# Kernel optimization log

Hardware: AMD Instinct MI355X
Metric: run time of the kernel (lower is better)

Reference implementation:

```python
import jax, jax.numpy as jnp
import numpy as np

PAD_IDX = 0
K = 5
TEMPERATURE = 1.0
BATCH = 256
VOCAB = 50257


def setup_inputs() -> dict:
    key = jax.random.key(0)
    k1, k2, k3, k4, k5 = jax.random.split(key, 5)
    draft_tokens = jax.random.randint(k1, (BATCH, K), 0, VOCAB)
    # valid-ish log-probabilities (negative values)
    draft_log_probs = -jax.random.uniform(k2, (BATCH, K), minval=0.05, maxval=8.0, dtype=jnp.float32)
    target_logits = jax.random.normal(k3, (BATCH, K, VOCAB), dtype=jnp.float32)
    random_vals = jax.random.uniform(k4, (BATCH, K), dtype=jnp.float32)
    uniform_sample = jax.random.uniform(k5, (BATCH,), dtype=jnp.float32)
    return {
        "draft_tokens": draft_tokens,
        "draft_log_probs": draft_log_probs,
        "target_logits": target_logits,
        "random_vals": random_vals,
        "uniform_sample": uniform_sample,
    }


def reference(draft_tokens, draft_log_probs, target_logits, random_vals, uniform_sample):
    B, k = draft_tokens.shape
    # --- accept/reject scan ---
    tlp = jax.nn.log_softmax(target_logits / TEMPERATURE, axis=-1)          # [B,k,V]
    tlp_draft = jnp.take_along_axis(tlp, draft_tokens[..., None], axis=2)[..., 0]  # [B,k]
    accept_probs = jnp.minimum(jnp.exp(tlp_draft - draft_log_probs), 1.0)
    accepted_mask = random_vals < accept_probs
    rejected_sent = jnp.concatenate(
        [~accepted_mask, jnp.ones((B, 1), dtype=bool)], axis=1)              # [B,k+1]
    first_reject = jnp.argmax(rejected_sent, axis=1)                         # [B]
    n_accepted = first_reject
    # fixed-width (k) accepted_tokens, PAD-filled past n_accepted (jit-friendly
    # variant of torch's dynamic max_accepted truncation; same valid entries)
    pos = jnp.arange(k)[None, :]
    accepted_tokens = jnp.where(pos < n_accepted[:, None], draft_tokens, PAD_IDX)
    # --- vectorized fallback sampling at first reject position ---
    rp = jnp.minimum(first_reject, k - 1)                                    # clamp for gather
    sel_logits = jnp.take_along_axis(target_logits, rp[:, None, None], axis=1)[:, 0, :]  # [B,V]
    target_probs = jax.nn.softmax(sel_logits / TEMPERATURE, axis=-1)
    dlp_sel = jnp.take_along_axis(draft_log_probs, rp[:, None], axis=1)      # [B,1]
    # torch builds a constant vector exp(dlp) over the whole vocab
    draft_probs = jnp.exp(dlp_sel)                                           # [B,1] broadcasts
    adjusted = jnp.clip(target_probs - draft_probs, 0.0)
    s = adjusted.sum(axis=-1, keepdims=True)
    probs = jnp.where(s > 0, adjusted / jnp.where(s > 0, s, 1.0), target_probs)  # [B,V]
    # multinomial(probs, 1) via inverse CDF with provided uniform sample
    cdf = jnp.cumsum(probs, axis=-1)
    thresh = uniform_sample[:, None] * cdf[:, -1:]
    sampled = jnp.argmax(cdf >= thresh, axis=-1)                             # [B]
    final_tokens = jnp.where(first_reject < k, sampled, PAD_IDX)
    return accepted_tokens, n_accepted, final_tokens
```

## Files before the change

### kernel.cpp

```cpp
#include <hip/hip_runtime.h>
#include <math.h>
#include <stdint.h>

#define VOCAB 50257
#define KD 5
#define NBATCH 256
#define NT 1024
#define NW (NT / 64)
#define NSLOT 13
#define NSEG (NSLOT + 2)

__global__ __launch_bounds__(NT) void spec_decode_kernel(
    const int* __restrict__ dtok,
    const float* __restrict__ dlp,
    const float* __restrict__ logits,
    const float* __restrict__ rnd,
    const float* __restrict__ usmp,
    int* __restrict__ out)
{
    const int b    = blockIdx.x;
    const int tid  = threadIdx.x;
    const int lane = tid & 63;
    const int wv   = tid >> 6;

    __shared__ double s_w[NW];
    __shared__ double s_pA[NSLOT][NW + 1];
    __shared__ double s_pR[NSLOT][NW + 1];
    __shared__ double s_ht[6];
    __shared__ double s_db[2];
    __shared__ int    s_ib[2];
    __shared__ int    s_c[NW];

    float ef[NSLOT][4];

    double       Zsel  = 0.0;
    int          n_acc = KD;
    int          headS = 0, nvecS = 0;
    const float* rowS  = nullptr;

    for (int r = 0; r < KD; ++r) {
        const float* row = logits + ((size_t)b * KD + r) * (size_t)VOCAB;
        const int  head = (int)((4u - ((((uintptr_t)row) >> 2) & 3u)) & 3u);
        const int  nvec = (VOCAB - head) >> 2;
        const float4* row4 = (const float4*)(row + head);

        float tlogit = 0.f, dl = 0.f, rv = 0.f;
        if (tid == 0) {
            int tok = dtok[b * KD + r];
            tlogit  = row[tok];
            dl      = dlp[b * KD + r];
            rv      = rnd[b * KD + r];
        }

        double l0 = 0.0, l1 = 0.0;
        if (tid < head) {
            double eh = (double)expf(row[tid]);
            l0 += eh;
            s_ht[tid] = eh;
        }
        #pragma unroll
        for (int c = 0; c < NSLOT - 1; ++c) {
            float4 x = row4[c * NT + tid];
            float e0 = expf(x.x), e1 = expf(x.y), e2 = expf(x.z), e3 = expf(x.w);
            ef[c][0] = e0; ef[c][1] = e1; ef[c][2] = e2; ef[c][3] = e3;
            l0 += (double)e0 + (double)e1;
            l1 += (double)e2 + (double)e3;
        }
        {
            int i = (NSLOT - 1) * NT + tid;
            if (i < nvec) {
                float4 x = row4[i];
                float e0 = expf(x.x), e1 = expf(x.y), e2 = expf(x.z), e3 = expf(x.w);
                ef[NSLOT - 1][0] = e0; ef[NSLOT - 1][1] = e1;
                ef[NSLOT - 1][2] = e2; ef[NSLOT - 1][3] = e3;
                l0 += (double)e0 + (double)e1;
                l1 += (double)e2 + (double)e3;
            }
        }
        const int tail_start = head + (nvec << 2);
        const int tail_cnt   = VOCAB - tail_start;
        if (tid < tail_cnt) {
            double et = (double)expf(row[tail_start + tid]);
            l1 += et;
            s_ht[3 + tid] = et;
        }

        double local = l0 + l1;
        for (int off = 32; off; off >>= 1) local += __shfl_down(local, off, 64);
        if (lane == 0) s_w[wv] = local;
        __syncthreads();
        if (wv == 0) {
            double v = (lane < NW) ? s_w[lane] : 0.0;
            for (int off = 8; off; off >>= 1) v += __shfl_down(v, off, 64);
            if (lane == 0) {
                double Z   = v;
                double tlp = (double)tlogit - log(Z);
                double ap  = exp(tlp - (double)dl);
                if (ap > 1.0) ap = 1.0;
                s_db[0] = Z;
                s_ib[0] = ((double)rv < ap) ? 1 : 0;
            }
        }
        __syncthreads();
        Zsel  = s_db[0];
        int acc = s_ib[0];
        headS = head; nvecS = nvec; rowS = row;
        if (!acc) { n_acc = r; break; }
    }

    if (tid == 0) {
        for (int r = 0; r < KD; ++r)
            out[b * KD + r] = (r < n_acc) ? dtok[b * KD + r] : 0;
        out[NBATCH * KD + b] = n_acc;
        if (n_acc >= KD) out[NBATCH * KD + NBATCH + b] = 0;
    }
    if (n_acc >= KD) return;

    const double invZ = 1.0 / Zsel;
    const double dp   = exp((double)dlp[b * KD + n_acc]);
    const int    head = headS;
    const int    nvec = nvecS;
    const float4* row4 = (const float4*)(rowS + head);

    #pragma unroll
    for (int c = 0; c < NSLOT; ++c) {
        double aS = 0.0, rS = 0.0;
        bool v = (c < NSLOT - 1) || ((NSLOT - 1) * NT + tid < nvec);
        if (v) {
            #pragma unroll
            for (int e = 0; e < 4; ++e) {
                double p = (double)ef[c][e] * invZ;
                rS += p;
                double a = p - dp;
                if (a > 0.0) aS += a;
            }
        }
        for (int off = 32; off; off >>= 1) {
            aS += __shfl_down(aS, off, 64);
            rS += __shfl_down(rS, off, 64);
        }
        if (lane == 0) { s_pA[c][wv] = aS; s_pR[c][wv] = rS; }
    }
    __syncthreads();

    if (wv == 0) {
        double A = 0.0, R = 0.0;
        if (lane >= 1 && lane <= NSLOT) {
            #pragma unroll
            for (int w = 0; w < NW; ++w) { A += s_pA[lane - 1][w]; R += s_pR[lane - 1][w]; }
        } else if (lane == 0) {
            for (int j = 0; j < head; ++j) {
                double p = s_ht[j] * invZ;
                R += p;
                double a = p - dp; if (a > 0.0) A += a;
            }
        } else if (lane == NSEG - 1) {
            int tcnt = VOCAB - head - (nvec << 2);
            for (int j = 0; j < tcnt; ++j) {
                double p = s_ht[3 + j] * invZ;
                R += p;
                double a = p - dp; if (a > 0.0) A += a;
            }
        }
        double sa = A, sr = R;
        for (int off = 1; off < 16; off <<= 1) {
            double va = __shfl_up(sa, (unsigned)off, 64); if (lane >= off) sa += va;
            double vr = __shfl_up(sr, (unsigned)off, 64); if (lane >= off) sr += vr;
        }
        double SA     = __shfl(sa, NSEG - 1, 64);
        int    useAdj = (SA > 0.0) ? 1 : 0;
        double Tot    = useAdj ? SA : __shfl(sr, NSEG - 1, 64);
        double T      = (double)usmp[b] * Tot;
        double incl   = useAdj ? sa : sr;
        double val    = useAdj ? A  : R;
        bool crossed  = (lane < NSEG) && (incl >= T);
        unsigned long long mk = __ballot(crossed);
        int    cseg = mk ? (int)(__ffsll(mk) - 1) : (NSEG - 1);
        double Pex  = __shfl(incl, cseg, 64) - __shfl(val, cseg, 64);
        if (lane == 0) {
            s_db[0] = Pex; s_db[1] = T;
            s_ib[0] = cseg; s_ib[1] = useAdj;
        }
    }
    __syncthreads();

    const double P      = s_db[0];
    const double T      = s_db[1];
    const int    cseg   = s_ib[0];
    const int    useAdj = s_ib[1];

    if (cseg >= 1 && cseg <= NSLOT) {
        const int  c     = cseg - 1;
        const int  i4    = c * NT + tid;
        const bool valid = i4 < nvec;
        double c0 = 0, c1 = 0, c2 = 0, c3 = 0, tsum = 0;
        if (valid) {
            float4 x = row4[i4];
            double p0 = (double)expf(x.x) * invZ;
            double p1 = (double)expf(x.y) * invZ;
            double p2 = (double)expf(x.z) * invZ;
            double p3 = (double)expf(x.w) * invZ;
            double g0 = useAdj ? fmax(p0 - dp, 0.0) : p0;
            double g1 = useAdj ? fmax(p1 - dp, 0.0) : p1;
            double g2 = useAdj ? fmax(p2 - dp, 0.0) : p2;
            double g3 = useAdj ? fmax(p3 - dp, 0.0) : p3;
            c0 = g0; c1 = c0 + g1; c2 = c1 + g2; c3 = c2 + g3;
            tsum = c3;
        }
        double sc = tsum;
        for (int off = 1; off < 64; off <<= 1) {
            double v = __shfl_up(sc, (unsigned)off, 64);
            if (lane >= off) sc += v;
        }
        if (lane == 63) s_w[wv] = sc;
        __syncthreads();
        double woff = 0.0;
        for (int w = 0; w < wv; ++w) woff += s_w[w];
        double base = P + woff + (sc - tsum);
        int bj = -1;
        if (valid) {
            if      (base + c0 >= T) bj = 0;
            else if (base + c1 >= T) bj = 1;
            else if (base + c2 >= T) bj = 2;
            else if (base + c3 >= T) bj = 3;
        }
        unsigned long long mk = __ballot(bj >= 0);
        int L  = mk ? (int)(__ffsll(mk) - 1) : 0;
        int jl = __shfl(bj, L, 64);
        if (lane == 0)
            s_c[wv] = mk ? (head + 4 * (c * NT + wv * 64 + L) + jl) : 0x7FFFFFFF;
        __syncthreads();
        if (tid == 0) {
            int best = 0x7FFFFFFF;
            for (int w = 0; w < NW; ++w) best = min(best, s_c[w]);
            int smp;
            if (best == 0x7FFFFFFF) {
                int endv = c * NT + NT; if (endv > nvec) endv = nvec;
                smp = head + 4 * endv - 1;
            } else {
                smp = best;
            }
            out[NBATCH * KD + NBATCH + b] = smp;
        }
    } else if (tid == 0) {
        int smp = -1;
        if (cseg == 0) {
            double cum = P;
            for (int j = 0; j < head; ++j) {
                double p = s_ht[j] * invZ;
                double g = useAdj ? fmax(p - dp, 0.0) : p;
                cum += g;
                if (cum >= T) { smp = j; break; }
            }
            if (smp < 0) smp = (head > 0) ? head - 1 : 0;
        } else {
            int ts   = head + (nvec << 2);
            int tcnt = VOCAB - ts;
            double cum = P;
            for (int j = 0; j < tcnt; ++j) {
                double p = s_ht[3 + j] * invZ;
                double g = useAdj ? fmax(p - dp, 0.0) : p;
                cum += g;
                if (cum >= T) { smp = ts + j; break; }
            }
            if (smp < 0) smp = VOCAB - 1;
        }
        out[NBATCH * KD + NBATCH + b] = smp;
    }
}

extern "C" void kernel_launch(void* const* d_in, const int* in_sizes, int n_in,
                              void* d_out, int out_size, void* d_ws, size_t ws_size,
                              hipStream_t stream) {
    const int*   dtok   = (const int*)d_in[0];
    const float* dlp    = (const float*)d_in[1];
    const float* logits = (const float*)d_in[2];
    const float* rnd    = (const float*)d_in[3];
    const float* usmp   = (const float*)d_in[4];
    int*         out    = (int*)d_out;
    (void)in_sizes; (void)n_in; (void)out_size; (void)d_ws; (void)ws_size;
    spec_decode_kernel<<<dim3(NBATCH), dim3(NT), 0, stream>>>(
        dtok, dlp, logits, rnd, usmp, out);
}
```

Measured before the change: 340.5 us.

## Drop register-cached exps, track row max to skip adjusted pass when unused

```diff
diff --git a/kernel.cpp b/kernel.cpp
--- a/kernel.cpp
+++ b/kernel.cpp
@@ -23,15 +23,14 @@
     const int lane = tid & 63;
     const int wv   = tid >> 6;
 
-    __shared__ double s_w[NW];
+    __shared__ double s_pR[NSLOT][NW + 1];
     __shared__ double s_pA[NSLOT][NW + 1];
-    __shared__ double s_pR[NSLOT][NW + 1];
     __shared__ double s_ht[6];
+    __shared__ float  s_mx[NW];
+    __shared__ float  s_emax;
     __shared__ double s_db[2];
     __shared__ int    s_ib[2];
-    __shared__ int    s_c[NW];
-
-    float ef[NSLOT][4];
+    __shared__ double s_w[NW];
 
     double       Zsel  = 0.0;
     int          n_acc = KD;
@@ -42,6 +41,7 @@
         const float* row = logits + ((size_t)b * KD + r) * (size_t)VOCAB;
         const int  head = (int)((4u - ((((uintptr_t)row) >> 2) & 3u)) & 3u);
         const int  nvec = (VOCAB - head) >> 2;
+        const int  tail_start = head + (nvec << 2);
         const float4* row4 = (const float4*)(row + head);
 
         float tlogit = 0.f, dl = 0.f, rv = 0.f;
@@ -52,46 +52,48 @@
             rv      = rnd[b * KD + r];
         }
 
-        double l0 = 0.0, l1 = 0.0;
+        float mx = 0.0f;
         if (tid < head) {
-            double eh = (double)expf(row[tid]);
-            l0 += eh;
-            s_ht[tid] = eh;
+            float e = expf(row[tid]);
+            s_ht[tid] = (double)e;
+            mx = fmaxf(mx, e);
+        }
+        if (tid < VOCAB - tail_start) {
+            float e = expf(row[tail_start + tid]);
+            s_ht[3 + tid] = (double)e;
+            mx = fmaxf(mx, e);
         }
         #pragma unroll
-        for (int c = 0; c < NSLOT - 1; ++c) {
-            float4 x = row4[c * NT + tid];
-            float e0 = expf(x.x), e1 = expf(x.y), e2 = expf(x.z), e3 = expf(x.w);
-            ef[c][0] = e0; ef[c][1] = e1; ef[c][2] = e2; ef[c][3] = e3;
-            l0 += (double)e0 + (double)e1;
-            l1 += (double)e2 + (double)e3;
-        }
-        {
-            int i = (NSLOT - 1) * NT + tid;
-            if (i < nvec) {
+        for (int c = 0; c < NSLOT; ++c) {
+            double sl = 0.0;
+            const int i = c * NT + tid;
+            if (c < NSLOT - 1 || i < nvec) {
                 float4 x = row4[i];
                 float e0 = expf(x.x), e1 = expf(x.y), e2 = expf(x.z), e3 = expf(x.w);
-                ef[NSLOT - 1][0] = e0; ef[NSLOT - 1][1] = e1;
-                ef[NSLOT - 1][2] = e2; ef[NSLOT - 1][3] = e3;
-                l0 += (double)e0 + (double)e1;
-                l1 += (double)e2 + (double)e3;
-            }
-        }
-        const int tail_start = head + (nvec << 2);
-        const int tail_cnt   = VOCAB - tail_start;
-        if (tid < tail_cnt) {
-            double et = (double)expf(row[tail_start + tid]);
-            l1 += et;
-            s_ht[3 + tid] = et;
-        }
-
-        double local = l0 + l1;
-        for (int off = 32; off; off >>= 1) local += __shfl_down(local, off, 64);
-        if (lane == 0) s_w[wv] = local;
-        __syncthreads();
+                mx = fmaxf(fmaxf(mx, fmaxf(e0, e1)), fmaxf(e2, e3));
+                sl = ((double)e0 + (double)e1) + ((double)e2 + (double)e3);
+            }
+            for (int off = 32; off; off >>= 1) sl += __shfl_down(sl, off, 64);
+            if (lane == 0) s_pR[c][wv] = sl;
+        }
+        for (int off = 32; off; off >>= 1) mx = fmaxf(mx, __shfl_down(mx, off, 64));
+        if (lane == 0) s_mx[wv] = mx;
+        __syncthreads();
+
         if (wv == 0) {
-            double v = (lane < NW) ? s_w[lane] : 0.0;
-            for (int off = 8; off; off >>= 1) v += __shfl_down(v, off, 64);
+            double v = 0.0;
+            if (lane < NSLOT * (NW / 4)) {
+                int c = lane >> 2, w0 = (lane & 3) << 2;
+                v = (s_pR[c][w0] + s_pR[c][w0 + 1]) + (s_pR[c][w0 + 2] + s_pR[c][w0 + 3]);
+            } else if (lane == 52) {
+                for (int j = 0; j < head; ++j) v += s_ht[j];
+            } else if (lane == 53) {
+                int tcnt = VOCAB - tail_start;
+                for (int j = 0; j < tcnt; ++j) v += s_ht[3 + j];
+            }
+            for (int off = 32; off; off >>= 1) v += __shfl_down(v, off, 64);
+            float m = (lane < NW) ? s_mx[lane] : 0.0f;
+            for (int off = 8; off; off >>= 1) m = fmaxf(m, __shfl_down(m, off, 64));
             if (lane == 0) {
                 double Z   = v;
                 double tlp = (double)tlogit - log(Z);
@@ -99,6 +101,7 @@
                 if (ap > 1.0) ap = 1.0;
                 s_db[0] = Z;
                 s_ib[0] = ((double)rv < ap) ? 1 : 0;
+                s_emax  = m;
             }
         }
         __syncthreads();
@@ -121,73 +124,75 @@
     const int    head = headS;
     const int    nvec = nvecS;
     const float4* row4 = (const float4*)(rowS + head);
-
-    #pragma unroll
-    for (int c = 0; c < NSLOT; ++c) {
-        double aS = 0.0, rS = 0.0;
-        bool v = (c < NSLOT - 1) || ((NSLOT - 1) * NT + tid < nvec);
-        if (v) {
-            #pragma unroll
-            for (int e = 0; e < 4; ++e) {
-                double p = (double)ef[c][e] * invZ;
-                rS += p;
-                double a = p - dp;
-                if (a > 0.0) aS += a;
-            }
-        }
-        for (int off = 32; off; off >>= 1) {
-            aS += __shfl_down(aS, off, 64);
-            rS += __shfl_down(rS, off, 64);
-        }
-        if (lane == 0) { s_pA[c][wv] = aS; s_pR[c][wv] = rS; }
+    const int useAdj = ((double)s_emax * invZ > dp) ? 1 : 0;
+
+    if (useAdj) {
+        #pragma unroll
+        for (int c = 0; c < NSLOT; ++c) {
+            double aS = 0.0;
+            const int i = c * NT + tid;
+            if (c < NSLOT - 1 || i < nvec) {
+                float4 x = row4[i];
+                double p0 = (double)expf(x.x) * invZ;
+                double p1 = (double)expf(x.y) * invZ;
+                double p2 = (double)expf(x.z) * invZ;
+                double p3 = (double)expf(x.w) * invZ;
+                double a0 = p0 - dp; if (a0 > 0.0) aS += a0;
+                double a1 = p1 - dp; if (a1 > 0.0) aS += a1;
+                double a2 = p2 - dp; if (a2 > 0.0) aS += a2;
+                double a3 = p3 - dp; if (a3 > 0.0) aS += a3;
+            }
+            for (int off = 32; off; off >>= 1) aS += __shfl_down(aS, off, 64);
+            if (lane == 0) s_pA[c][wv] = aS;
+        }
     }
     __syncthreads();
 
     if (wv == 0) {
-        double A = 0.0, R = 0.0;
+        double X = 0.0;
         if (lane >= 1 && lane <= NSLOT) {
-            #pragma unroll
-            for (int w = 0; w < NW; ++w) { A += s_pA[lane - 1][w]; R += s_pR[lane - 1][w]; }
+            if (useAdj) {
+                #pragma unroll
+                for (int w = 0; w < NW; ++w) X += s_pA[lane - 1][w];
+            } else {
+                double t = 0.0;
+                #pragma unroll
+                for (int w = 0; w < NW; ++w) t += s_pR[lane - 1][w];
+                X = t * invZ;
+            }
         } else if (lane == 0) {
             for (int j = 0; j < head; ++j) {
                 double p = s_ht[j] * invZ;
-                R += p;
-                double a = p - dp; if (a > 0.0) A += a;
+                X += useAdj ? fmax(p - dp, 0.0) : p;
             }
         } else if (lane == NSEG - 1) {
             int tcnt = VOCAB - head - (nvec << 2);
             for (int j = 0; j < tcnt; ++j) {
                 double p = s_ht[3 + j] * invZ;
-                R += p;
-                double a = p - dp; if (a > 0.0) A += a;
-            }
-        }
-        double sa = A, sr = R;
+                X += useAdj ? fmax(p - dp, 0.0) : p;
+            }
+        }
+        double sx = X;
         for (int off = 1; off < 16; off <<= 1) {
-            double va = __shfl_up(sa, (unsigned)off, 64); if (lane >= off) sa += va;
-            double vr = __shfl_up(sr, (unsigned)off, 64); if (lane >= off) sr += vr;
-        }
-        double SA     = __shfl(sa, NSEG - 1, 64);
-        int    useAdj = (SA > 0.0) ? 1 : 0;
-        double Tot    = useAdj ? SA : __shfl(sr, NSEG - 1, 64);
-        double T      = (double)usmp[b] * Tot;
-        double incl   = useAdj ? sa : sr;
-        double val    = useAdj ? A  : R;
-        bool crossed  = (lane < NSEG) && (incl >= T);
+            double vv = __shfl_up(sx, (unsigned)off, 64);
+            if (lane >= off) sx += vv;
+        }
+        double Tot = __shfl(sx, NSEG - 1, 64);
+        double T   = (double)usmp[b] * Tot;
+        bool crossed = (lane < NSEG) && (sx >= T);
         unsigned long long mk = __ballot(crossed);
         int    cseg = mk ? (int)(__ffsll(mk) - 1) : (NSEG - 1);
-        double Pex  = __shfl(incl, cseg, 64) - __shfl(val, cseg, 64);
+        double Pex  = __shfl(sx, cseg, 64) - __shfl(X, cseg, 64);
         if (lane == 0) {
             s_db[0] = Pex; s_db[1] = T;
-            s_ib[0] = cseg; s_ib[1] = useAdj;
+            s_ib[0] = cseg;
         }
     }
     __syncthreads();
 
-    const double P      = s_db[0];
-    const double T      = s_db[1];
-    const int    cseg   = s_ib[0];
-    const int    useAdj = s_ib[1];
+    const double P    = s_db[0];
+    const double T    = s_db[1];
+    const int    cseg = s_ib[0];
 
     if (cseg >= 1 && cseg <= NSLOT) {
         const int  c     = cseg - 1;
@@ -227,6 +232,7 @@
         unsigned long long mk = __ballot(bj >= 0);
         int L  = mk ? (int)(__ffsll(mk) - 1) : 0;
         int jl = __shfl(bj, L, 64);
+        __shared__ int s_c[NW];
         if (lane == 0)
             s_c[wv] = mk ? (head + 4 * (c * NT + wv * 64 + L) + jl) : 0x7FFFFFFF;
         __syncthreads();
```

Measured after the change: 321.0 us. 1.06x faster.
